# Kernel tuning notes

Measured on AMD Instinct MI355X. Metric: run time of the kernel, lower is better.

## Reference

```python
import jax, jax.numpy as jnp
import numpy as np

B, N, H, W = 2, 65536, 256, 256
FEA, OUT, CMP, MAX_PT = 8, 512, 32, 64
EPS = 1e-5


def _xavier(key, fan_in, fan_out):
    scale = np.sqrt(2.0 / (fan_in + fan_out)).astype(np.float32)
    return jax.random.normal(key, (fan_in, fan_out), dtype=jnp.float32) * scale


def setup_inputs() -> dict:
    key = jax.random.key(0)
    ks = jax.random.split(key, 8)
    pt_fea = jax.random.normal(ks[0], (B, N, FEA), dtype=jnp.float32)
    xy_ind = jax.random.randint(ks[1], (B, N, 2), 0, H, dtype=jnp.int32)
    return {
        "pt_fea": pt_fea,
        "bn0_g": jnp.ones((FEA,), jnp.float32), "bn0_b": jnp.zeros((FEA,), jnp.float32),
        "W1": _xavier(ks[2], FEA, 64),
        "bn1_g": jnp.ones((64,), jnp.float32), "bn1_b": jnp.zeros((64,), jnp.float32),
        "W2": _xavier(ks[3], 64, 128),
        "bn2_g": jnp.ones((128,), jnp.float32), "bn2_b": jnp.zeros((128,), jnp.float32),
        "W3": _xavier(ks[4], 128, 256),
        "bn3_g": jnp.ones((256,), jnp.float32), "bn3_b": jnp.zeros((256,), jnp.float32),
        "W4": _xavier(ks[5], 256, OUT),
        "Wc": _xavier(ks[6], OUT, CMP),
        "xy_ind": xy_ind,
    }


def _forward(pt_fea, bn0_g, bn0_b, W1, bn1_g, bn1_b, W2, bn2_g, bn2_b,
             W3, bn3_g, bn3_b, W4, Wc, xy_ind):
    Bc, Nc, Fc = pt_fea.shape
    P = Bc * Nc
    feats = pt_fea.reshape(P, Fc)
    batch_id = jnp.repeat(jnp.arange(Bc, dtype=jnp.int32), Nc)
    xy = xy_ind.reshape(P, 2)
    keys = batch_id * (H * W) + xy[:, 0] * W + xy[:, 1]  # linearized voxel id

    # random shuffle of points (torch.randperm)
    perm = jax.random.permutation(jax.random.key(42), P)
    feats = feats[perm]
    keys = keys[perm]

    # rank of each point within its voxel, in shuffled order
    # (== grp_range_torch(unq_cnt)[argsort(argsort(unq_inv))])
    order = jnp.argsort(keys)  # stable
    sk = keys[order]
    pos = jnp.arange(P)
    new_grp = jnp.concatenate([jnp.array([True]), sk[1:] != sk[:-1]])
    grp_start = jax.lax.cummax(jnp.where(new_grp, pos, 0))
    rank = jnp.zeros(P, jnp.int32).at[order].set((pos - grp_start).astype(jnp.int32))
    mask = rank < MAX_PT  # keep at most MAX_PT points per voxel

    # PPmodel: BN -> Lin -> BN -> ReLU x3 -> Lin, BN stats over kept points only
    m = mask[:, None].astype(feats.dtype)
    cnt = jnp.sum(m)

    def bn(x, g, b):
        mu = jnp.sum(x * m, axis=0) / cnt
        var = jnp.sum(jnp.square(x - mu) * m, axis=0) / cnt  # biased var
        return (x - mu) * jax.lax.rsqrt(var + EPS) * g + b

    x = bn(feats, bn0_g, bn0_b)
    x = jax.nn.relu(bn(x @ W1, bn1_g, bn1_b))
    x = jax.nn.relu(bn(x @ W2, bn2_g, bn2_b))
    x = jax.nn.relu(bn(x @ W3, bn3_g, bn3_b))
    x = x @ W4  # [P, OUT]

    # scatter_max segment reduction into dense voxel grid
    NEG = jnp.finfo(x.dtype).min
    x = jnp.where(mask[:, None], x, NEG)
    S = Bc * H * W
    pooled = jax.ops.segment_max(x, keys, num_segments=S)
    occupied = jax.ops.segment_sum(jnp.ones(P, x.dtype), keys, num_segments=S) > 0
    pooled = jnp.where(occupied[:, None], pooled, 0.0)

    comp = jax.nn.relu(pooled @ Wc)  # fea_compression
    comp = jnp.where(occupied[:, None], comp, 0.0)  # empty voxels stay zero
    out = comp.reshape(Bc, H, W, CMP).transpose(0, 3, 1, 2)  # [B, C, H, W]
    return out


def reference(pt_fea, bn0_g, bn0_b, W1, bn1_g, bn1_b, W2, bn2_g, bn2_b,
              W3, bn3_g, bn3_b, W4, Wc, xy_ind):
    return _forward(pt_fea, bn0_g, bn0_b, W1, bn1_g, bn1_b, W2, bn2_g, bn2_b,
                    W3, bn3_g, bn3_b, W4, Wc, xy_ind)
```

## Files before the change

### kernel.cpp

```cpp
#include <hip/hip_runtime.h>
#include <cstdint>
#include <cstddef>


#define P_TOT  131072
#define HWSZ   65536
#define WGRID  256
#define S_TOT  131072
#define EPS    1e-5f
#define CNTF   131072.0f

#define OFF_Y3    0ull
#define OFF_Y1    67108864ull
#define OFF_Y2    100663296ull
#define OFF_POOL  67108864ull
#define OFF_CNT   201326592ull
#define OFF_ST    201850880ull
#define OFF_OFFS  201916416ull
#define OFF_CUR   202440704ull
#define OFF_BSUM  202964992ull
#define OFF_PIDF  202969088ull
#define OFF_SEND  203493376ull
#define OFF_SKEY  204017664ull
#define OFF_W3F   204541952ull
#define OFF_W4F   204607488ull
#define OFF_WCF   204869632ull
#define OFF_W2F   204902400ull
#define OFF_SCSH  204918784ull

typedef __attribute__((ext_vector_type(8)))  short bf16x8;
typedef __attribute__((ext_vector_type(16))) float f32x16;

__device__ __forceinline__ unsigned f2bf(float f) {
    unsigned u = __float_as_uint(f);
    return (u + 0x7FFFu + ((u >> 16) & 1u)) >> 16;
}
__device__ __forceinline__ float bf2f(unsigned h) {
    return __uint_as_float(h << 16);
}

__global__ __launch_bounds__(256) void k_zero(uint4* __restrict__ p, int n_u4) {
    int i = blockIdx.x * blockDim.x + threadIdx.x;
    if (i < n_u4) p[i] = make_uint4(0u, 0u, 0u, 0u);
}

__global__ __launch_bounds__(256) void k_prepw(
    const float* __restrict__ W2, const float* __restrict__ W3,
    const float* __restrict__ W4, const float* __restrict__ Wc,
    uint4* __restrict__ W2F, uint4* __restrict__ W3F,
    uint4* __restrict__ W4F, uint4* __restrict__ WcF)
{
    int gw = (blockIdx.x * 256 + threadIdx.x) >> 6;
    int l = threadIdx.x & 63;
    const float* W; uint4* dst; int M, mt, ks, fi;
    if (gw < 64)       { fi = gw;       W = W3; dst = W3F; M = 256; mt = fi >> 3; ks = fi & 7;  }
    else if (gw < 320) { fi = gw - 64;  W = W4; dst = W4F; M = 512; mt = fi >> 4; ks = fi & 15; }
    else if (gw < 352) { fi = gw - 320; W = Wc; dst = WcF; M = 32;  mt = 0;      ks = fi;      }
    else               { fi = gw - 352; W = W2; dst = W2F; M = 128; mt = fi >> 2; ks = fi & 3;  }
    int m = mt * 32 + (l & 31);
    int k0 = ks * 16 + (l >> 5) * 8;
    unsigned p[4];
    #pragma unroll
    for (int jj = 0; jj < 4; ++jj) {
        unsigned lo = f2bf(W[(size_t)(k0 + 2*jj)     * M + m]);
        unsigned hi = f2bf(W[(size_t)(k0 + 2*jj + 1) * M + m]);
        p[jj] = lo | (hi << 16);
    }
    dst[(size_t)fi * 64 + l] = make_uint4(p[0], p[1], p[2], p[3]);
}

__global__ __launch_bounds__(256) void k_bnprep(
    const float* __restrict__ st, const float* __restrict__ g,
    const float* __restrict__ b, float* __restrict__ sc,
    float* __restrict__ sh, int nch)
{
    int c = blockIdx.x * 256 + threadIdx.x;
    if (c >= nch) return;
    float mu = st[c * 16] * (1.0f / CNTF);
    float var = st[(nch + c) * 16] * (1.0f / CNTF) - mu * mu;
    float rs = rsqrtf(var + EPS);
    float s = rs * g[c];
    sc[c] = s;
    sh[c] = b[c] - mu * s;
}

__global__ __launch_bounds__(256) void k_fold(
    unsigned short* __restrict__ y, const float* __restrict__ sc,
    const float* __restrict__ sh, int nch, int n_u4)
{
    int i = blockIdx.x * 256 + threadIdx.x;
    if (i >= n_u4) return;
    int ch0 = (i * 8) & (nch - 1);
    float4 s0 = *(const float4*)(sc + ch0), s1 = *(const float4*)(sc + ch0 + 4);
    float4 h0 = *(const float4*)(sh + ch0), h1 = *(const float4*)(sh + ch0 + 4);
    float scv[8] = {s0.x,s0.y,s0.z,s0.w,s1.x,s1.y,s1.z,s1.w};
    float shv[8] = {h0.x,h0.y,h0.z,h0.w,h1.x,h1.y,h1.z,h1.w};
    uint4 e = ((const uint4*)y)[i];
    unsigned eu[4] = {e.x, e.y, e.z, e.w};
    unsigned ou[4];
    #pragma unroll
    for (int jj = 0; jj < 4; ++jj) {
        float x0 = fmaxf(fmaf(bf2f(eu[jj] & 0xFFFFu), scv[2*jj],   shv[2*jj]),   0.f);
        float x1 = fmaxf(fmaf(bf2f(eu[jj] >> 16),     scv[2*jj+1], shv[2*jj+1]), 0.f);
        ou[jj] = f2bf(x0) | (f2bf(x1) << 16);
    }
    ((uint4*)y)[i] = make_uint4(ou[0], ou[1], ou[2], ou[3]);
}

__global__ __launch_bounds__(256) void k_stats0(
    const float* __restrict__ pt, const int* __restrict__ xy,
    float* __restrict__ st0, unsigned* __restrict__ counts)
{
    __shared__ float part[4][16];
    const int tid = threadIdx.x;
    const int p = blockIdx.x * 256 + tid;
    const float4* f4 = (const float4*)(pt + (size_t)p * 8);
    float4 a = f4[0], b = f4[1];
    float v[8] = {a.x,a.y,a.z,a.w,b.x,b.y,b.z,b.w};
    int key = (p >> 16) * HWSZ + xy[2*p] * WGRID + xy[2*p + 1];
    atomicAdd(&counts[key], 1u);
    float s[8], q[8];
    #pragma unroll
    for (int k = 0; k < 8; ++k) { s[k] = v[k]; q[k] = v[k]*v[k]; }
    #pragma unroll
    for (int k = 0; k < 8; ++k) {
        #pragma unroll
        for (int off = 32; off > 0; off >>= 1) {
            s[k] += __shfl_down(s[k], off);
            q[k] += __shfl_down(q[k], off);
        }
    }
    if ((tid & 63) == 0) {
        int w = tid >> 6;
        #pragma unroll
        for (int k = 0; k < 8; ++k) { part[w][k] = s[k]; part[w][8 + k] = q[k]; }
    }
    __syncthreads();
    if (tid < 16) {
        float t = part[0][tid] + part[1][tid] + part[2][tid] + part[3][tid];
        atomicAdd(&st0[tid * 16], t);
    }
}

__global__ __launch_bounds__(256) void k_lin1(
    const float* __restrict__ pt, const float* __restrict__ g0,
    const float* __restrict__ b0, const float* __restrict__ W1,
    const float* __restrict__ st0, float* __restrict__ y1,
    float* __restrict__ st1)
{
    __shared__ float x0s[64 * 8];
    __shared__ float w1s[8 * 64];
    __shared__ float sc0s[8], sh0s[8];
    __shared__ float red[256];
    const int tid = threadIdx.x;

    if (tid < 8) {
        float mu = st0[tid * 16] * (1.0f / CNTF);
        float var = st0[(8 + tid) * 16] * (1.0f / CNTF) - mu * mu;
        float rs = rsqrtf(var + EPS);
        sc0s[tid] = rs * g0[tid];
        sh0s[tid] = b0[tid] - mu * rs * g0[tid];
    }
    if (tid < 128) ((float4*)w1s)[tid] = ((const float4*)W1)[tid];
    const int c = tid & 63;
    const int psub = tid >> 6;
    float ssum = 0.f, ssq = 0.f;
    for (int t = 0; t < 4; ++t) {
        const int pbase = blockIdx.x * 256 + t * 64;
        __syncthreads();
        if (tid < 128) {
            float4 f = ((const float4*)(pt + (size_t)pbase * 8))[tid];
            int cc = (tid & 1) * 4;
            f.x = fmaf(f.x, sc0s[cc + 0], sh0s[cc + 0]);
            f.y = fmaf(f.y, sc0s[cc + 1], sh0s[cc + 1]);
            f.z = fmaf(f.z, sc0s[cc + 2], sh0s[cc + 2]);
            f.w = fmaf(f.w, sc0s[cc + 3], sh0s[cc + 3]);
            ((float4*)x0s)[tid] = f;
        }
        __syncthreads();
        #pragma unroll
        for (int i = 0; i < 16; ++i) {
            int pl = psub * 16 + i;
            float acc = 0.f;
            #pragma unroll
            for (int k = 0; k < 8; ++k)
                acc = fmaf(x0s[pl * 8 + k], w1s[k * 64 + c], acc);
            y1[(size_t)(pbase + pl) * 64 + c] = acc;
            ssum += acc; ssq += acc * acc;
        }
    }
    red[tid] = ssum; __syncthreads();
    if (tid < 64) atomicAdd(&st1[tid * 16],
        red[tid] + red[tid+64] + red[tid+128] + red[tid+192]);
    __syncthreads();
    red[tid] = ssq; __syncthreads();
    if (tid < 64) atomicAdd(&st1[(64 + tid) * 16],
        red[tid] + red[tid+64] + red[tid+128] + red[tid+192]);
}

__global__ __launch_bounds__(256) void k_scan1(
    const unsigned* __restrict__ counts, unsigned* __restrict__ bsum)
{
    __shared__ unsigned sh[256];
    int t = threadIdx.x;
    sh[t] = counts[blockIdx.x * 256 + t];
    __syncthreads();
    for (int d = 128; d > 0; d >>= 1) {
        if (t < d) sh[t] += sh[t + d];
        __syncthreads();
    }
    if (t == 0) bsum[blockIdx.x] = sh[0];
}

__global__ __launch_bounds__(256) void k_scan2(
    const unsigned* __restrict__ bsum, unsigned* __restrict__ boff)
{
    __shared__ unsigned sh[256];
    int t = threadIdx.x;
    unsigned a = bsum[2*t], b = bsum[2*t+1];
    unsigned s = a + b;
    sh[t] = s; __syncthreads();
    for (int d = 1; d < 256; d <<= 1) {
        unsigned u = (t >= d) ? sh[t-d] : 0u;
        __syncthreads();
        sh[t] += u;
        __syncthreads();
    }
    unsigned excl = sh[t] - s;
    boff[2*t]   = excl;
    boff[2*t+1] = excl + a;
}

__global__ __launch_bounds__(256) void k_scan3(
    const unsigned* __restrict__ counts, const unsigned* __restrict__ boff,
    unsigned* __restrict__ offs)
{
    __shared__ unsigned sh[256];
    int t = threadIdx.x, b = blockIdx.x;
    unsigned v = counts[b*256 + t];
    sh[t] = v; __syncthreads();
    for (int d = 1; d < 256; d <<= 1) {
        unsigned u = (t >= d) ? sh[t-d] : 0u;
        __syncthreads();
        sh[t] += u;
        __syncthreads();
    }
    offs[b*256 + t] = boff[b] + sh[t] - v;
}

__global__ __launch_bounds__(256) void k_fill(
    const int* __restrict__ xy, const unsigned* __restrict__ offs,
    const unsigned* __restrict__ counts, unsigned* __restrict__ cur,
    unsigned* __restrict__ pidf, unsigned* __restrict__ send,
    unsigned* __restrict__ skey)
{
    int p = blockIdx.x * 256 + threadIdx.x;
    int key = (p >> 16) * HWSZ + xy[2*p] * WGRID + xy[2*p + 1];
    unsigned o = offs[key];
    unsigned r = atomicAdd(&cur[key], 1u);
    unsigned slot = o + r;
    pidf[slot] = (unsigned)p | (r == 0 ? 0x80000000u : 0u);
    send[slot] = o + counts[key];
    skey[slot] = (unsigned)key;
}

__global__ __launch_bounds__(256, 2) void k_lin2(
    const float* __restrict__ y1, const float* __restrict__ g1,
    const float* __restrict__ b1, const uint4* __restrict__ W2F,
    const float* __restrict__ st1, unsigned short* __restrict__ y2,
    float* __restrict__ st2)
{
    __shared__ uint4 w2s[1024];
    __shared__ float sc1s[64], sh1s[64];
    const int tid = threadIdx.x, l = tid & 63, w = tid >> 6;
    if (tid < 64) {
        float mu = st1[tid * 16] * (1.0f / CNTF);
        float var = st1[(64 + tid) * 16] * (1.0f / CNTF) - mu * mu;
        float rs = rsqrtf(var + EPS);
        sc1s[tid] = rs * g1[tid];
        sh1s[tid] = b1[tid] - mu * rs * g1[tid];
    }
    #pragma unroll
    for (int r = 0; r < 4; ++r) w2s[r * 256 + tid] = W2F[r * 256 + tid];
    __syncthreads();
    const int n = l & 31, q = l >> 5;
    float s_acc[16], q_acc[16];
    #pragma unroll
    for (int r = 0; r < 16; ++r) { s_acc[r] = 0.f; q_acc[r] = 0.f; }

    for (int t = 0; t < 8; ++t) {
        const int p = (blockIdx.x * 8 + t) * 32 + n;
        const float* yrow = y1 + (size_t)p * 64 + q * 8;
        bf16x8 Bf[4];
        #pragma unroll
        for (int ks = 0; ks < 4; ++ks) {
            float4 v0 = *(const float4*)(yrow + ks * 16);
            float4 v1 = *(const float4*)(yrow + ks * 16 + 4);
            int k0 = ks * 16 + q * 8;
            float e[8] = {v0.x,v0.y,v0.z,v0.w,v1.x,v1.y,v1.z,v1.w};
            union { bf16x8 v; unsigned u[4]; } cv;
            #pragma unroll
            for (int jj = 0; jj < 4; ++jj) {
                float a0 = fmaxf(fmaf(e[2*jj],   sc1s[k0+2*jj],   sh1s[k0+2*jj]),   0.f);
                float a1 = fmaxf(fmaf(e[2*jj+1], sc1s[k0+2*jj+1], sh1s[k0+2*jj+1]), 0.f);
                cv.u[jj] = f2bf(a0) | (f2bf(a1) << 16);
            }
            Bf[ks] = cv.v;
        }
        f32x16 acc;
        #pragma unroll
        for (int r = 0; r < 16; ++r) acc[r] = 0.f;
        #pragma unroll
        for (int ks = 0; ks < 4; ++ks) {
            union { uint4 u; bf16x8 v; } av;
            av.u = w2s[(w * 4 + ks) * 64 + l];
            acc = __builtin_amdgcn_mfma_f32_32x32x16_bf16(av.v, Bf[ks], acc, 0, 0, 0);
        }
        #pragma unroll
        for (int g = 0; g < 4; ++g) {
            int ch0 = w * 32 + 8 * g + 4 * q;
            ushort4 pk;
            pk.x = (unsigned short)f2bf(acc[4*g+0]);
            pk.y = (unsigned short)f2bf(acc[4*g+1]);
            pk.z = (unsigned short)f2bf(acc[4*g+2]);
            pk.w = (unsigned short)f2bf(acc[4*g+3]);
            *(ushort4*)(y2 + (size_t)p * 128 + ch0) = pk;
        }
        #pragma unroll
        for (int r = 0; r < 16; ++r) { s_acc[r] += acc[r]; q_acc[r] += acc[r]*acc[r]; }
    }
    #pragma unroll
    for (int r = 0; r < 16; ++r) {
        float s = s_acc[r], sq = q_acc[r];
        #pragma unroll
        for (int off = 16; off > 0; off >>= 1) {
            s  += __shfl_xor(s, off);
            sq += __shfl_xor(sq, off);
        }
        if ((l & 31) == 0) {
            int ch = w * 32 + (r & 3) + 8 * (r >> 2) + 4 * q;
            atomicAdd(&st2[ch * 16], s);
            atomicAdd(&st2[(128 + ch) * 16], sq);
        }
    }
}

__global__ __launch_bounds__(256, 2) void k_lin3(
    const unsigned short* __restrict__ y2f, const uint4* __restrict__ W3F,
    unsigned short* __restrict__ y3, float* __restrict__ st3)
{
    __shared__ uint4 w3s[4096];
    const int tid = threadIdx.x, l = tid & 63, w = tid >> 6;
    #pragma unroll
    for (int r = 0; r < 16; ++r) w3s[r * 256 + tid] = W3F[r * 256 + tid];
    __syncthreads();
    const int n = l & 31, q = l >> 5;
    float s_acc[32], q_acc[32];
    #pragma unroll
    for (int r = 0; r < 32; ++r) { s_acc[r] = 0.f; q_acc[r] = 0.f; }

    for (int t = 0; t < 8; ++t) {
        const int p = (blockIdx.x * 8 + t) * 32 + n;
        const unsigned short* yrow = y2f + (size_t)p * 128 + q * 8;
        bf16x8 Bf[8];
        #pragma unroll
        for (int ks = 0; ks < 8; ++ks) {
            union { uint4 u; bf16x8 v; } bv;
            bv.u = *(const uint4*)(yrow + ks * 16);
            Bf[ks] = bv.v;
        }
        f32x16 acc[2];
        #pragma unroll
        for (int i = 0; i < 2; ++i)
            #pragma unroll
            for (int r = 0; r < 16; ++r) acc[i][r] = 0.f;
        #pragma unroll
        for (int ks = 0; ks < 8; ++ks) {
            #pragma unroll
            for (int i = 0; i < 2; ++i) {
                union { uint4 u; bf16x8 v; } av;
                av.u = w3s[((w * 2 + i) * 8 + ks) * 64 + l];
                acc[i] = __builtin_amdgcn_mfma_f32_32x32x16_bf16(av.v, Bf[ks], acc[i], 0, 0, 0);
            }
        }
        #pragma unroll
        for (int i = 0; i < 2; ++i) {
            #pragma unroll
            for (int g = 0; g < 4; ++g) {
                int ch0 = (w * 2 + i) * 32 + 8 * g + 4 * q;
                ushort4 pk;
                pk.x = (unsigned short)f2bf(acc[i][4*g+0]);
                pk.y = (unsigned short)f2bf(acc[i][4*g+1]);
                pk.z = (unsigned short)f2bf(acc[i][4*g+2]);
                pk.w = (unsigned short)f2bf(acc[i][4*g+3]);
                *(ushort4*)(y3 + (size_t)p * 256 + ch0) = pk;
            }
            #pragma unroll
            for (int r = 0; r < 16; ++r) {
                s_acc[i*16+r] += acc[i][r];
                q_acc[i*16+r] += acc[i][r] * acc[i][r];
            }
        }
    }
    #pragma unroll
    for (int i = 0; i < 2; ++i)
        #pragma unroll
        for (int r = 0; r < 16; ++r) {
            float s = s_acc[i*16+r], sq = q_acc[i*16+r];
            #pragma unroll
            for (int off = 16; off > 0; off >>= 1) {
                s  += __shfl_xor(s, off);
                sq += __shfl_xor(sq, off);
            }
            if ((l & 31) == 0) {
                int ch = (w * 2 + i) * 32 + (r & 3) + 8 * (r >> 2) + 4 * q;
                atomicAdd(&st3[ch * 16], s);
                atomicAdd(&st3[(256 + ch) * 16], sq);
            }
        }
}

__global__ __launch_bounds__(256, 2) void k_smax(
    const unsigned short* __restrict__ y3f, const uint4* __restrict__ W4F,
    const unsigned* __restrict__ pidf, const unsigned* __restrict__ send,
    const unsigned* __restrict__ skey, unsigned short* __restrict__ pooled)
{
    const int tid = threadIdx.x, l = tid & 63, w = tid >> 6;
    const int ms = blockIdx.x & 3;
    const int wg = blockIdx.x >> 2;
    const int q = l >> 5;
    const int nt = ms * 4 + w;

    uint4 Wf[16];
    #pragma unroll
    for (int ks = 0; ks < 16; ++ks)
        Wf[ks] = W4F[(size_t)(nt * 16 + ks) * 64 + l];

    float s0c = -3.4e38f;
    for (int t = 8; t >= 0; --t) {
        const int p0 = (wg * 8 + t) * 32;
        int pos = p0 + (l & 31);
        int sp = pos < P_TOT ? pos : P_TOT - 1;
        unsigned pf = pidf[sp];
        unsigned e_l = send[sp];
        unsigned key_l = skey[sp];
        const unsigned short* row =
            y3f + (size_t)(pf & 0x7FFFFFFFu) * 256 + q * 8;
        f32x16 acc;
        #pragma unroll
        for (int r = 0; r < 16; ++r) acc[r] = 0.f;
        #pragma unroll
        for (int ks = 0; ks < 16; ++ks) {
            union { uint4 u; bf16x8 v; } xv;
            xv.u = *(const uint4*)(row + ks * 16);
            union { uint4 u; bf16x8 v; } wv;
            wv.u = Wf[ks];
            acc = __builtin_amdgcn_mfma_f32_32x32x16_bf16(xv.v, wv.v, acc, 0, 0, 0);
        }
        float v[32];
        #pragma unroll
        for (int r = 0; r < 16; ++r) {
            int base = (r & 3) + 8 * (r >> 2);
            float o = __shfl_xor(acc[r], 32);
            v[base]     = q ? o : acc[r];
            v[base + 4] = q ? acc[r] : o;
        }
        {
            unsigned em = (unsigned)__builtin_amdgcn_readlane((int)e_l, 31);
            if ((unsigned)(p0 + 32) < em) v[31] = fmaxf(v[31], s0c);
        }
        #pragma unroll
        for (int m = 30; m >= 0; --m) {
            unsigned em = (unsigned)__builtin_amdgcn_readlane((int)e_l, m);
            if ((unsigned)(p0 + m + 1) < em) v[m] = fmaxf(v[m], v[m + 1]);
        }
        s0c = v[0];
        if (t < 8) {
            #pragma unroll
            for (int m = 0; m < 32; ++m) {
                int fm = __builtin_amdgcn_readlane((int)pf, m);
                if (fm < 0) {
                    unsigned km = (unsigned)__builtin_amdgcn_readlane((int)key_l, m);
                    if ((m >> 4) == q)
                        pooled[(size_t)km * 512 + nt * 32 + (l & 31)] =
                            (unsigned short)f2bf(v[m]);
                }
            }
        }
    }
}

__global__ __launch_bounds__(256, 4) void k_out(
    const unsigned short* __restrict__ pooled, const unsigned* __restrict__ counts,
    const uint4* __restrict__ WcF, float* __restrict__ out)
{
    __shared__ uint4 wcs[2048];
    const int tid = threadIdx.x, l = tid & 63, w = tid >> 6;
    const int sbase = blockIdx.x * 128;
    #pragma unroll
    for (int r = 0; r < 8; ++r) wcs[r * 256 + tid] = WcF[r * 256 + tid];
    __syncthreads();
    const int n = l & 31, q = l >> 5;
    const int s = sbase + w * 32 + n;
    const unsigned short* prow = pooled + (size_t)s * 512 + q * 8;
    f32x16 acc;
    #pragma unroll
    for (int r = 0; r < 16; ++r) acc[r] = 0.f;

    for (int ks = 0; ks < 32; ++ks) {
        union { uint4 u; bf16x8 v; } bv;
        bv.u = *(const uint4*)(prow + ks * 16);
        union { uint4 u; bf16x8 v; } av;
        av.u = wcs[ks * 64 + l];
        acc = __builtin_amdgcn_mfma_f32_32x32x16_bf16(av.v, bv.v, acc, 0, 0, 0);
    }
    const bool occ = counts[s] > 0;
    const int b = s >> 16, hw = s & 65535;
    #pragma unroll
    for (int r = 0; r < 16; ++r) {
        int ch = (r & 3) + 8 * (r >> 2) + 4 * q;
        float x = occ ? fmaxf(acc[r], 0.f) : 0.f;
        out[(size_t)b * (32 * HWSZ) + (size_t)ch * HWSZ + hw] = x;
    }
}

extern "C" void kernel_launch(void* const* d_in, const int* in_sizes, int n_in,
                              void* d_out, int out_size, void* d_ws, size_t ws_size,
                              hipStream_t stream) {
    const float* pt = (const float*)d_in[0];
    const float* g0 = (const float*)d_in[1];
    const float* b0 = (const float*)d_in[2];
    const float* W1 = (const float*)d_in[3];
    const float* g1 = (const float*)d_in[4];
    const float* b1 = (const float*)d_in[5];
    const float* W2 = (const float*)d_in[6];
    const float* g2 = (const float*)d_in[7];
    const float* b2 = (const float*)d_in[8];
    const float* W3 = (const float*)d_in[9];
    const float* g3 = (const float*)d_in[10];
    const float* b3 = (const float*)d_in[11];
    const float* W4 = (const float*)d_in[12];
    const float* Wc = (const float*)d_in[13];
    const int*   xy = (const int*)d_in[14];
    float* out = (float*)d_out;

    char* ws = (char*)d_ws;
    unsigned short* y3     = (unsigned short*)(ws + OFF_Y3);
    float*          y1     = (float*)(ws + OFF_Y1);
    unsigned short* y2     = (unsigned short*)(ws + OFF_Y2);
    unsigned short* pool16 = (unsigned short*)(ws + OFF_POOL);
    unsigned*       counts = (unsigned*)(ws + OFF_CNT);
    float*          st     = (float*)(ws + OFF_ST);
    unsigned*       offs   = (unsigned*)(ws + OFF_OFFS);
    unsigned*       cur    = (unsigned*)(ws + OFF_CUR);
    unsigned*       bsum   = (unsigned*)(ws + OFF_BSUM);
    unsigned*       pidf   = (unsigned*)(ws + OFF_PIDF);
    unsigned*       send   = (unsigned*)(ws + OFF_SEND);
    unsigned*       skey   = (unsigned*)(ws + OFF_SKEY);
    uint4* W3F = (uint4*)(ws + OFF_W3F);
    uint4* W4F = (uint4*)(ws + OFF_W4F);
    uint4* WcF = (uint4*)(ws + OFF_WCF);
    uint4* W2F = (uint4*)(ws + OFF_W2F);
    float* scsh = (float*)(ws + OFF_SCSH);
    float* sc2 = scsh;       float* sh2 = scsh + 128;
    float* sc3 = scsh + 256; float* sh3 = scsh + 512;
    float* st0 = st;
    float* st1 = st + 256;
    float* st2 = st + 2304;
    float* st3 = st + 6400;

    k_zero<<<400, 256, 0, stream>>>((uint4*)(ws + OFF_CNT), 102400);
    k_prepw<<<92, 256, 0, stream>>>(W2, W3, W4, Wc, W2F, W3F, W4F, WcF);

    k_stats0<<<512, 256, 0, stream>>>(pt, xy, st0, counts);
    k_scan1<<<512, 256, 0, stream>>>(counts, bsum);
    k_scan2<<<1,   256, 0, stream>>>(bsum, bsum + 512);
    k_scan3<<<512, 256, 0, stream>>>(counts, bsum + 512, offs);
    k_fill<<<512, 256, 0, stream>>>(xy, offs, counts, cur, pidf, send, skey);

    k_lin1<<<512, 256, 0, stream>>>(pt, g0, b0, W1, st0, y1, st1);
    k_lin2<<<512, 256, 0, stream>>>(y1, g1, b1, W2F, st1, y2, st2);
    k_bnprep<<<1, 256, 0, stream>>>(st2, g2, b2, sc2, sh2, 128);
    k_fold<<<8192, 256, 0, stream>>>(y2, sc2, sh2, 128, 2097152);
    k_lin3<<<512, 256, 0, stream>>>(y2, W3F, y3, st3);
    k_bnprep<<<1, 256, 0, stream>>>(st3, g3, b3, sc3, sh3, 256);
    k_fold<<<16384, 256, 0, stream>>>(y3, sc3, sh3, 256, 4194304);

    k_smax<<<2048, 256, 0, stream>>>(y3, W4F, pidf, send, skey, pool16);
    k_out<<<S_TOT / 128, 256, 0, stream>>>(pool16, counts, WcF, out);
}
```

Baseline: 488.8 us.

## Reuse gathered point rows across all output tiles in scatter-max kernel

The scatter-max kernel now has each block loop over all four output-channel sub-tiles. Each gathered y3 row is loaded once into registers and reused, where before four separate blocks each re-gathered it. W4 fragments are now streamed from global memory per sub-tile instead of held in registers. The per-element readlane checks are replaced by ballot masks, and the flush loop iterates only over set bits. The output kernel redirects reads for empty voxels to row 0 to avoid touching uninitialized pooled memory. The trade-off is 4x fewer blocks with more serial work per block, plus extra weight-load traffic.

```diff
diff --git a/kernel.cpp b/kernel.cpp
--- a/kernel.cpp
+++ b/kernel.cpp
@@ -426,60 +426,60 @@
     const unsigned* __restrict__ skey, unsigned short* __restrict__ pooled)
 {
     const int tid = threadIdx.x, l = tid & 63, w = tid >> 6;
-    const int ms = blockIdx.x & 3;
-    const int wg = blockIdx.x >> 2;
+    const int wg = blockIdx.x;
     const int q = l >> 5;
-    const int nt = ms * 4 + w;
-
-    uint4 Wf[16];
-    #pragma unroll
-    for (int ks = 0; ks < 16; ++ks)
-        Wf[ks] = W4F[(size_t)(nt * 16 + ks) * 64 + l];
-
-    float s0c = -3.4e38f;
+
+    float s0c[4] = {-3.4e38f, -3.4e38f, -3.4e38f, -3.4e38f};
+    #pragma unroll 1
     for (int t = 8; t >= 0; --t) {
         const int p0 = (wg * 8 + t) * 32;
-        int pos = p0 + (l & 31);
-        int sp = pos < P_TOT ? pos : P_TOT - 1;
-        unsigned pf = pidf[sp];
-        unsigned e_l = send[sp];
-        unsigned key_l = skey[sp];
+        const int pos = p0 + (l & 31);
+        const int sp = pos < P_TOT ? pos : P_TOT - 1;
+        const unsigned pf = pidf[sp];
+        const unsigned e_l = send[sp];
+        const unsigned key_l = skey[sp];
+        const unsigned cmask =
+            (unsigned)__ballot((unsigned)(pos + 1) < e_l);
+        const unsigned fmask =
+            (unsigned)__ballot((pf & 0x80000000u) != 0u);
         const unsigned short* row =
             y3f + (size_t)(pf & 0x7FFFFFFFu) * 256 + q * 8;
-        f32x16 acc;
-        #pragma unroll
-        for (int r = 0; r < 16; ++r) acc[r] = 0.f;
-        #pragma unroll
-        for (int ks = 0; ks < 16; ++ks) {
-            union { uint4 u; bf16x8 v; } xv;
-            xv.u = *(const uint4*)(row + ks * 16);
-            union { uint4 u; bf16x8 v; } wv;
-            wv.u = Wf[ks];
-            acc = __builtin_amdgcn_mfma_f32_32x32x16_bf16(xv.v, wv.v, acc, 0, 0, 0);
-        }
-        float v[32];
-        #pragma unroll
-        for (int r = 0; r < 16; ++r) {
-            int base = (r & 3) + 8 * (r >> 2);
-            float o = __shfl_xor(acc[r], 32);
-            v[base]     = q ? o : acc[r];
-            v[base + 4] = q ? acc[r] : o;
-        }
-        {
-            unsigned em = (unsigned)__builtin_amdgcn_readlane((int)e_l, 31);
-            if ((unsigned)(p0 + 32) < em) v[31] = fmaxf(v[31], s0c);
-        }
-        #pragma unroll
-        for (int m = 30; m >= 0; --m) {
-            unsigned em = (unsigned)__builtin_amdgcn_readlane((int)e_l, m);
-            if ((unsigned)(p0 + m + 1) < em) v[m] = fmaxf(v[m], v[m + 1]);
-        }
-        s0c = v[0];
-        if (t < 8) {
-            #pragma unroll
-            for (int m = 0; m < 32; ++m) {
-                int fm = __builtin_amdgcn_readlane((int)pf, m);
-                if (fm < 0) {
+        uint4 Xf[16];
+        #pragma unroll
+        for (int ks = 0; ks < 16; ++ks)
+            Xf[ks] = *(const uint4*)(row + ks * 16);
+
+        #pragma unroll 1
+        for (int sub = 0; sub < 4; ++sub) {
+            const int nt = sub * 4 + w;
+            f32x16 acc;
+            #pragma unroll
+            for (int r = 0; r < 16; ++r) acc[r] = 0.f;
+            #pragma unroll
+            for (int ks = 0; ks < 16; ++ks) {
+                union { uint4 u; bf16x8 v; } xv, wv;
+                xv.u = Xf[ks];
+                wv.u = W4F[(size_t)(nt * 16 + ks) * 64 + l];
+                acc = __builtin_amdgcn_mfma_f32_32x32x16_bf16(xv.v, wv.v, acc, 0, 0, 0);
+            }
+            float v[32];
+            #pragma unroll
+            for (int r = 0; r < 16; ++r) {
+                int base = (r & 3) + 8 * (r >> 2);
+                float o = __shfl_xor(acc[r], 32);
+                v[base]     = q ? o : acc[r];
+                v[base + 4] = q ? acc[r] : o;
+            }
+            if ((cmask >> 31) & 1) v[31] = fmaxf(v[31], s0c[sub]);
+            #pragma unroll
+            for (int m = 30; m >= 0; --m)
+                if ((cmask >> m) & 1) v[m] = fmaxf(v[m], v[m + 1]);
+            s0c[sub] = v[0];
+            if (t < 8) {
+                unsigned fm = fmask;
+                while (fm) {
+                    int m = __ffs(fm) - 1;
+                    fm &= fm - 1;
                     unsigned km = (unsigned)__builtin_amdgcn_readlane((int)key_l, m);
                     if ((m >> 4) == q)
                         pooled[(size_t)km * 512 + nt * 32 + (l & 31)] =
@@ -502,7 +502,9 @@
     __syncthreads();
     const int n = l & 31, q = l >> 5;
     const int s = sbase + w * 32 + n;
-    const unsigned short* prow = pooled + (size_t)s * 512 + q * 8;
+    const bool occ = counts[s] > 0;
+    const unsigned short* prow =
+        pooled + (occ ? (size_t)s * 512 : (size_t)0) + q * 8;
     f32x16 acc;
     #pragma unroll
     for (int r = 0; r < 16; ++r) acc[r] = 0.f;
@@ -514,7 +516,6 @@
         av.u = wcs[ks * 64 + l];
         acc = __builtin_amdgcn_mfma_f32_32x32x16_bf16(av.v, bv.v, acc, 0, 0, 0);
     }
-    const bool occ = counts[s] > 0;
     const int b = s >> 16, hw = s & 65535;
     #pragma unroll
     for (int r = 0; r < 16; ++r) {
@@ -586,6 +587,6 @@
     k_bnprep<<<1, 256, 0, stream>>>(st3, g3, b3, sc3, sh3, 256);
     k_fold<<<16384, 256, 0, stream>>>(y3, sc3, sh3, 256, 4194304);
 
-    k_smax<<<2048, 256, 0, stream>>>(y3, W4F, pidf, send, skey, pool16);
+    k_smax<<<512, 256, 0, stream>>>(y3, W4F, pidf, send, skey, pool16);
     k_out<<<S_TOT / 128, 256, 0, stream>>>(pool16, counts, WcF, out);
 }
```

Result: faster. 462.3 us (-5.4%).
